# Optimization experiments

Hardware: AMD Instinct MI355X
Metric: run time of the kernel (lower is better)

## Reference

```python
import jax, jax.numpy as jnp
import numpy as np

B = 2_097_152          # batch of theta samples
POLY_DEG = 127         # QSP polynomial degree -> 128 phases
PI = np.float32(np.pi)


def setup_inputs() -> dict:
    key = jax.random.key(0)
    k1, k2 = jax.random.split(key)
    th = jax.random.uniform(k1, (B, 1), dtype=jnp.float32) * PI
    phis = jax.random.uniform(k2, (POLY_DEG + 1, 1), dtype=jnp.float32) * PI
    return {"th": th, "phis": phis}


def reference(th, phis):
    # th: [B,1] float32, phis: [P+1,1] float32 (learned QSP phases)
    theta = th[:, 0]                      # [B]
    c = jnp.cos(theta)
    s = jnp.sin(theta)
    # expm(i*theta*X) = cos(theta) I + i sin(theta) X  (closed form, no expm)
    wx = jnp.stack(
        [jnp.stack([c + 0j, 1j * s], axis=-1),
         jnp.stack([1j * s, c + 0j], axis=-1)],
        axis=-2,
    ).astype(jnp.complex64)               # [B,2,2]

    phi = phis[:, 0]                      # [P+1]
    e = jnp.exp(1j * phi).astype(jnp.complex64)
    # expm(i*phi*Z) = diag(e^{i phi}, e^{-i phi})
    rz = (jnp.zeros((phi.shape[0], 2, 2), jnp.complex64)
          .at[:, 0, 0].set(e)
          .at[:, 1, 1].set(jnp.conj(e)))  # [P+1,2,2]

    u0 = jnp.broadcast_to(rz[0], (theta.shape[0], 2, 2))  # [B,2,2]

    def step(u, rzk):
        u = jnp.einsum('bij,bjk->bik', u, wx)   # u @ W(x)
        u = jnp.einsum('bij,jk->bik', u, rzk)   # ... @ Rz(phi_k)
        return u, None

    u, _ = jax.lax.scan(step, u0, rz[1:])       # 127 sequential steps
    # convention == 0: (Re[u_00], Im[u_00])
    return (jnp.real(u[:, 0, 0]), jnp.imag(u[:, 0, 0]))
```

## Files before the change

kernel.cpp:

```cpp
#include <hip/hip_runtime.h>


#define NPHI 128

__device__ __forceinline__ float wave_shr1(float x) {
    return __builtin_bit_cast(float,
        __builtin_amdgcn_update_dpp(0, __builtin_bit_cast(int, x),
                                    0x138, 0xf, 0xf, true));
}

__global__ __launch_bounds__(256, 4) void qsp_fused(
    const float* __restrict__ th,
    const float* __restrict__ phis,
    float* __restrict__ out,
    int Bq8)
{
    __shared__ alignas(16) float2 g2[NPHI];
    __shared__ float2 h[NPHI];

    const int tid = threadIdx.x;

    if (tid < 64) {
        const int L = tid;
        float sp, cp;
        __sincosf(phis[L], &sp, &cp);
        h[L] = make_float2(0.5f * cp, 0.5f * sp);
        __sincosf(phis[L + 64], &sp, &cp);
        h[L + 64] = make_float2(0.5f * cp, 0.5f * sp);

        float A0r = 0.f, A0i = 0.f, B0r = 0.f, B0i = 0.f;
        float A1r = 0.f, A1i = 0.f, B1r = 0.f, B1i = 0.f;
        const float2 h0 = h[0];
        if (L == 0) { A0r = 2.f * h0.x; A0i = 2.f * h0.y; }

        #pragma unroll 4
        for (int k = 1; k < NPHI; ++k) {
            const float2 hk = h[k];
            const float hx = hk.x, hy = hk.y;
            const float pAr = wave_shr1(A1r), pAi = wave_shr1(A1i);
            const float pBr = wave_shr1(B1r), pBi = wave_shr1(B1i);
            const float u0r = pAr + pBr, u0i = pAi + pBi;
            const float v0r = A0r - B0r, v0i = A0i - B0i;
            const float sA0r = u0r + v0r, sA0i = u0i + v0i;
            const float sB0r = u0r - v0r, sB0i = u0i - v0i;
            const float u1r = A0r + B0r, u1i = A0i + B0i;
            const float v1r = A1r - B1r, v1i = A1i - B1i;
            const float sA1r = u1r + v1r, sA1i = u1i + v1i;
            const float sB1r = u1r - v1r, sB1i = u1i - v1i;
            A0r = fmaf(hx, sA0r, -hy * sA0i);
            A0i = fmaf(hx, sA0i,  hy * sA0r);
            B0r = fmaf(hx, sB0r,  hy * sB0i);
            B0i = fmaf(hx, sB0i, -hy * sB0r);
            A1r = fmaf(hx, sA1r, -hy * sA1i);
            A1i = fmaf(hx, sA1i,  hy * sA1r);
            B1r = fmaf(hx, sB1r,  hy * sB1i);
            B1i = fmaf(hx, sB1i, -hy * sB1r);
        }
        ((float4*)g2)[L] = make_float4(A0r, A0i, A1r, A1i);
    }

    const int idx = blockIdx.x * blockDim.x + tid;
    const int lidx = (idx < Bq8) ? idx : 0;
    const float4 ta = ((const float4*)th)[2 * lidx];
    const float4 tb = ((const float4*)th)[2 * lidx + 1];
    const float th8[8] = {ta.x, ta.y, ta.z, ta.w, tb.x, tb.y, tb.z, tb.w};

    float zr[8], zi[8];
    #pragma unroll
    for (int e = 0; e < 8; ++e) {
        float s, c;
        __sincosf(2.f * th8[e], &s, &c);
        zr[e] = c; zi[e] = s;
    }

    __syncthreads();

    float ar[8], ai[8];
    #pragma unroll
    for (int e = 0; e < 8; ++e) { ar[e] = 0.f; ai[e] = 0.f; }

    const float4* g4 = (const float4*)g2;
    float4 gp = g4[NPHI / 2 - 1];

    #pragma unroll 4
    for (int jj = NPHI / 2 - 1; jj >= 1; --jj) {
        const float4 gn = g4[jj - 1];
        #pragma unroll
        for (int e = 0; e < 8; ++e) {
            const float nr = fmaf(ar[e], zr[e], fmaf(-ai[e], zi[e], gp.z));
            const float ni = fmaf(ar[e], zi[e], fmaf( ai[e], zr[e], gp.w));
            ar[e] = nr; ai[e] = ni;
        }
        #pragma unroll
        for (int e = 0; e < 8; ++e) {
            const float nr = fmaf(ar[e], zr[e], fmaf(-ai[e], zi[e], gp.x));
            const float ni = fmaf(ar[e], zi[e], fmaf( ai[e], zr[e], gp.y));
            ar[e] = nr; ai[e] = ni;
        }
        gp = gn;
    }
    #pragma unroll
    for (int e = 0; e < 8; ++e) {
        const float nr = fmaf(ar[e], zr[e], fmaf(-ai[e], zi[e], gp.z));
        const float ni = fmaf(ar[e], zi[e], fmaf( ai[e], zr[e], gp.w));
        ar[e] = nr; ai[e] = ni;
    }
    #pragma unroll
    for (int e = 0; e < 8; ++e) {
        const float nr = fmaf(ar[e], zr[e], fmaf(-ai[e], zi[e], gp.x));
        const float ni = fmaf(ar[e], zi[e], fmaf( ai[e], zr[e], gp.y));
        ar[e] = nr; ai[e] = ni;
    }

    float orv[8], oiv[8];
    #pragma unroll
    for (int e = 0; e < 8; ++e) {
        float S, C;
        __sincosf(127.f * th8[e], &S, &C);
        orv[e] = fmaf(ar[e], C,  ai[e] * S);
        oiv[e] = fmaf(ai[e], C, -ar[e] * S);
    }

    if (idx < Bq8) {
        float4* o4 = (float4*)out;
        const int ib = 2 * Bq8;
        o4[2 * idx]          = make_float4(orv[0], orv[1], orv[2], orv[3]);
        o4[2 * idx + 1]      = make_float4(orv[4], orv[5], orv[6], orv[7]);
        o4[ib + 2 * idx]     = make_float4(oiv[0], oiv[1], oiv[2], oiv[3]);
        o4[ib + 2 * idx + 1] = make_float4(oiv[4], oiv[5], oiv[6], oiv[7]);
    }
}

extern "C" void kernel_launch(void* const* d_in, const int* in_sizes, int n_in,
                              void* d_out, int out_size, void* d_ws, size_t ws_size,
                              hipStream_t stream)
{
    const float* th   = (const float*)d_in[0];
    const float* phis = (const float*)d_in[1];
    float* out = (float*)d_out;
    const int B = in_sizes[0];
    const int Bq8 = B >> 3;
    const int block = 256;
    const int grid = (Bq8 + block - 1) / block;
    qsp_fused<<<grid, block, 0, stream>>>(th, phis, out, Bq8);
}
```

Measured before the change: 86.53 us.

## Split coefficient precompute into separate kernel and read coefficients from global memory

The per-block recomputation of the polynomial coefficients (a serial 127-step wave loop in the first wave of every block, followed by __syncthreads) moves into a tiny one-wave kernel that writes them to workspace. The main kernel reads the coefficients straight from global memory, which should hit in cache as uniform loads, and no longer needs the block barrier. The Horner loop is restructured to process two float4 coefficient pairs per iteration with a sched_barrier and unroll 1. The cost is an extra kernel launch and its serial latency before the main kernel can start.

After: 89.18 us. 3.1% more time.

```diff
diff --git a/kernel.cpp b/kernel.cpp
--- a/kernel.cpp
+++ b/kernel.cpp
@@ -9,56 +9,56 @@
                                     0x138, 0xf, 0xf, true));
 }
 
-__global__ __launch_bounds__(256, 4) void qsp_fused(
+__global__ __launch_bounds__(64) void qsp_gamma(const float* __restrict__ phis,
+                                                float4* __restrict__ gout)
+{
+    __shared__ float2 h[NPHI];
+    const int L = threadIdx.x;
+
+    float sp, cp;
+    __sincosf(phis[L], &sp, &cp);
+    h[L] = make_float2(0.5f * cp, 0.5f * sp);
+    __sincosf(phis[L + 64], &sp, &cp);
+    h[L + 64] = make_float2(0.5f * cp, 0.5f * sp);
+
+    float A0r = 0.f, A0i = 0.f, B0r = 0.f, B0i = 0.f;
+    float A1r = 0.f, A1i = 0.f, B1r = 0.f, B1i = 0.f;
+    const float2 h0 = h[0];
+    if (L == 0) { A0r = 2.f * h0.x; A0i = 2.f * h0.y; }
+
+    #pragma unroll 4
+    for (int k = 1; k < NPHI; ++k) {
+        const float2 hk = h[k];
+        const float hx = hk.x, hy = hk.y;
+        const float pAr = wave_shr1(A1r), pAi = wave_shr1(A1i);
+        const float pBr = wave_shr1(B1r), pBi = wave_shr1(B1i);
+        const float u0r = pAr + pBr, u0i = pAi + pBi;
+        const float v0r = A0r - B0r, v0i = A0i - B0i;
+        const float sA0r = u0r + v0r, sA0i = u0i + v0i;
+        const float sB0r = u0r - v0r, sB0i = u0i - v0i;
+        const float u1r = A0r + B0r, u1i = A0i + B0i;
+        const float v1r = A1r - B1r, v1i = A1i - B1i;
+        const float sA1r = u1r + v1r, sA1i = u1i + v1i;
+        const float sB1r = u1r - v1r, sB1i = u1i - v1i;
+        A0r = fmaf(hx, sA0r, -hy * sA0i);
+        A0i = fmaf(hx, sA0i,  hy * sA0r);
+        B0r = fmaf(hx, sB0r,  hy * sB0i);
+        B0i = fmaf(hx, sB0i, -hy * sB0r);
+        A1r = fmaf(hx, sA1r, -hy * sA1i);
+        A1i = fmaf(hx, sA1i,  hy * sA1r);
+        B1r = fmaf(hx, sB1r,  hy * sB1i);
+        B1i = fmaf(hx, sB1i, -hy * sB1r);
+    }
+    gout[L] = make_float4(A0r, A0i, A1r, A1i);
+}
+
+__global__ __launch_bounds__(256, 4) void qsp_main(
     const float* __restrict__ th,
-    const float* __restrict__ phis,
+    const float4* __restrict__ g4,
     float* __restrict__ out,
     int Bq8)
 {
-    __shared__ alignas(16) float2 g2[NPHI];
-    __shared__ float2 h[NPHI];
-
     const int tid = threadIdx.x;
-
-    if (tid < 64) {
-        const int L = tid;
-        float sp, cp;
-        __sincosf(phis[L], &sp, &cp);
-        h[L] = make_float2(0.5f * cp, 0.5f * sp);
-        __sincosf(phis[L + 64], &sp, &cp);
-        h[L + 64] = make_float2(0.5f * cp, 0.5f * sp);
-
-        float A0r = 0.f, A0i = 0.f, B0r = 0.f, B0i = 0.f;
-        float A1r = 0.f, A1i = 0.f, B1r = 0.f, B1i = 0.f;
-        const float2 h0 = h[0];
-        if (L == 0) { A0r = 2.f * h0.x; A0i = 2.f * h0.y; }
-
-        #pragma unroll 4
-        for (int k = 1; k < NPHI; ++k) {
-            const float2 hk = h[k];
-            const float hx = hk.x, hy = hk.y;
-            const float pAr = wave_shr1(A1r), pAi = wave_shr1(A1i);
-            const float pBr = wave_shr1(B1r), pBi = wave_shr1(B1i);
-            const float u0r = pAr + pBr, u0i = pAi + pBi;
-            const float v0r = A0r - B0r, v0i = A0i - B0i;
-            const float sA0r = u0r + v0r, sA0i = u0i + v0i;
-            const float sB0r = u0r - v0r, sB0i = u0i - v0i;
-            const float u1r = A0r + B0r, u1i = A0i + B0i;
-            const float v1r = A1r - B1r, v1i = A1i - B1i;
-            const float sA1r = u1r + v1r, sA1i = u1i + v1i;
-            const float sB1r = u1r - v1r, sB1i = u1i - v1i;
-            A0r = fmaf(hx, sA0r, -hy * sA0i);
-            A0i = fmaf(hx, sA0i,  hy * sA0r);
-            B0r = fmaf(hx, sB0r,  hy * sB0i);
-            B0i = fmaf(hx, sB0i, -hy * sB0r);
-            A1r = fmaf(hx, sA1r, -hy * sA1i);
-            A1i = fmaf(hx, sA1i,  hy * sA1r);
-            B1r = fmaf(hx, sB1r,  hy * sB1i);
-            B1i = fmaf(hx, sB1i, -hy * sB1r);
-        }
-        ((float4*)g2)[L] = make_float4(A0r, A0i, A1r, A1i);
-    }
-
     const int idx = blockIdx.x * blockDim.x + tid;
     const int lidx = (idx < Bq8) ? idx : 0;
     const float4 ta = ((const float4*)th)[2 * lidx];
@@ -73,44 +73,37 @@
         zr[e] = c; zi[e] = s;
     }
 
-    __syncthreads();
-
     float ar[8], ai[8];
     #pragma unroll
     for (int e = 0; e < 8; ++e) { ar[e] = 0.f; ai[e] = 0.f; }
 
-    const float4* g4 = (const float4*)g2;
-    float4 gp = g4[NPHI / 2 - 1];
+    float4 gA = g4[62];
+    float4 gB = g4[63];
 
-    #pragma unroll 4
-    for (int jj = NPHI / 2 - 1; jj >= 1; --jj) {
-        const float4 gn = g4[jj - 1];
-        #pragma unroll
-        for (int e = 0; e < 8; ++e) {
-            const float nr = fmaf(ar[e], zr[e], fmaf(-ai[e], zi[e], gp.z));
-            const float ni = fmaf(ar[e], zi[e], fmaf( ai[e], zr[e], gp.w));
-            ar[e] = nr; ai[e] = ni;
+    #define QSP_STEP(gr, gi)                                                  \
+        _Pragma("unroll")                                                     \
+        for (int e = 0; e < 8; ++e) {                                         \
+            const float nr = fmaf(ar[e], zr[e], fmaf(-ai[e], zi[e], (gr)));   \
+            const float ni = fmaf(ar[e], zi[e], fmaf( ai[e], zr[e], (gi)));   \
+            ar[e] = nr; ai[e] = ni;                                           \
         }
-        #pragma unroll
-        for (int e = 0; e < 8; ++e) {
-            const float nr = fmaf(ar[e], zr[e], fmaf(-ai[e], zi[e], gp.x));
-            const float ni = fmaf(ar[e], zi[e], fmaf( ai[e], zr[e], gp.y));
-            ar[e] = nr; ai[e] = ni;
-        }
-        gp = gn;
+
+    #pragma unroll 1
+    for (int jj = 62; jj >= 2; jj -= 2) {
+        const float4 nA = g4[jj - 2];
+        const float4 nB = g4[jj - 1];
+        __builtin_amdgcn_sched_barrier(0);
+        QSP_STEP(gB.z, gB.w)
+        QSP_STEP(gB.x, gB.y)
+        QSP_STEP(gA.z, gA.w)
+        QSP_STEP(gA.x, gA.y)
+        gA = nA; gB = nB;
     }
-    #pragma unroll
-    for (int e = 0; e < 8; ++e) {
-        const float nr = fmaf(ar[e], zr[e], fmaf(-ai[e], zi[e], gp.z));
-        const float ni = fmaf(ar[e], zi[e], fmaf( ai[e], zr[e], gp.w));
-        ar[e] = nr; ai[e] = ni;
-    }
-    #pragma unroll
-    for (int e = 0; e < 8; ++e) {
-        const float nr = fmaf(ar[e], zr[e], fmaf(-ai[e], zi[e], gp.x));
-        const float ni = fmaf(ar[e], zi[e], fmaf( ai[e], zr[e], gp.y));
-        ar[e] = nr; ai[e] = ni;
-    }
+    QSP_STEP(gB.z, gB.w)
+    QSP_STEP(gB.x, gB.y)
+    QSP_STEP(gA.z, gA.w)
+    QSP_STEP(gA.x, gA.y)
+    #undef QSP_STEP
 
     float orv[8], oiv[8];
     #pragma unroll
@@ -142,5 +135,9 @@
     const int Bq8 = B >> 3;
     const int block = 256;
     const int grid = (Bq8 + block - 1) / block;
-    qsp_fused<<<grid, block, 0, stream>>>(th, phis, out, Bq8);
+
+    float4* gbuf = (float4*)d_ws;
+
+    qsp_gamma<<<1, 64, 0, stream>>>(phis, gbuf);
+    qsp_main<<<grid, block, 0, stream>>>(th, gbuf, out, Bq8);
 }
```
